# Kernel tuning notes

Measured on AMD Instinct MI355X. Metric: run time of the kernel, lower is better.

The kernel has to match this reference:

```python
import jax, jax.numpy as jnp
import numpy as np

N_NODES = 50000
IN_CH = 128
HID = 32
HEADS = 4
OUT_CH = 32
N_EDGES = 1600000
NEG_SLOPE = 0.2


def _gatv2(x, src, dst, Wl, bl, Wr, br, att, bias, H, C):
    """GATv2Conv (PyG semantics, add_self_loops already applied to src/dst).
    x: [N, F_in]; src/dst: [E]; Wl/Wr: [F_in, H*C]; att: [H, C]; bias: [H*C].
    Returns [N, H*C] (concat heads)."""
    N = x.shape[0]
    xl = (x @ Wl + bl).reshape(N, H, C)  # source-side transform
    xr = (x @ Wr + br).reshape(N, H, C)  # target-side transform
    e = jax.nn.leaky_relu(xl[src] + xr[dst], NEG_SLOPE)  # [E, H, C]
    logits = jnp.einsum('ehc,hc->eh', e, att)  # [E, H]
    # softmax over incoming edges of each target node (stable)
    m = jax.ops.segment_max(logits, dst, num_segments=N)[dst]
    p = jnp.exp(logits - m)
    denom = jax.ops.segment_sum(p, dst, num_segments=N)[dst]
    alpha = p / denom  # [E, H]
    out = jax.ops.segment_sum(alpha[:, :, None] * xl[src], dst, num_segments=N)
    return out.reshape(N, H * C) + bias


def setup_inputs() -> dict:
    key = jax.random.key(0)
    ks = jax.random.split(key, 16)
    s1 = 1.0 / np.sqrt(IN_CH)
    s2 = 1.0 / np.sqrt(HID * HEADS)
    inp = {
        'x': jax.random.normal(ks[0], (N_NODES, IN_CH), jnp.float32),
        'edge_index': jax.random.randint(ks[1], (2, N_EDGES), 0, N_NODES, jnp.int64 if jax.config.read('jax_enable_x64') else jnp.int32).astype(jnp.int32),
        # layer 1: in -> HID per head, HEADS heads
        'Wl1': jax.random.normal(ks[2], (IN_CH, HEADS * HID), jnp.float32) * s1,
        'bl1': jnp.zeros((HEADS * HID,), jnp.float32),
        'Wr1': jax.random.normal(ks[3], (IN_CH, HEADS * HID), jnp.float32) * s1,
        'br1': jnp.zeros((HEADS * HID,), jnp.float32),
        'att1': jax.random.normal(ks[4], (HEADS, HID), jnp.float32) * s1,
        'b1': jnp.zeros((HEADS * HID,), jnp.float32),
        # mu head: HID*HEADS -> OUT_CH, 1 head
        'Wl_mu': jax.random.normal(ks[5], (HEADS * HID, OUT_CH), jnp.float32) * s2,
        'bl_mu': jnp.zeros((OUT_CH,), jnp.float32),
        'Wr_mu': jax.random.normal(ks[6], (HEADS * HID, OUT_CH), jnp.float32) * s2,
        'br_mu': jnp.zeros((OUT_CH,), jnp.float32),
        'att_mu': jax.random.normal(ks[7], (1, OUT_CH), jnp.float32) * s2,
        'b_mu': jnp.zeros((OUT_CH,), jnp.float32),
        # logvar head
        'Wl_lv': jax.random.normal(ks[8], (HEADS * HID, OUT_CH), jnp.float32) * s2,
        'bl_lv': jnp.zeros((OUT_CH,), jnp.float32),
        'Wr_lv': jax.random.normal(ks[9], (HEADS * HID, OUT_CH), jnp.float32) * s2,
        'br_lv': jnp.zeros((OUT_CH,), jnp.float32),
        'att_lv': jax.random.normal(ks[10], (1, OUT_CH), jnp.float32) * s2,
        'b_lv': jnp.zeros((OUT_CH,), jnp.float32),
    }
    return inp


def reference(x, edge_index, Wl1, bl1, Wr1, br1, att1, b1,
              Wl_mu, bl_mu, Wr_mu, br_mu, att_mu, b_mu,
              Wl_lv, bl_lv, Wr_lv, br_lv, att_lv, b_lv):
    N = x.shape[0]
    loops = jnp.arange(N, dtype=edge_index.dtype)
    src = jnp.concatenate([edge_index[0], loops])  # add_self_loops=True
    dst = jnp.concatenate([edge_index[1], loops])
    h = jax.nn.relu(_gatv2(x, src, dst, Wl1, bl1, Wr1, br1, att1, b1, HEADS, HID))
    mu = _gatv2(h, src, dst, Wl_mu, bl_mu, Wr_mu, br_mu, att_mu, b_mu, 1, OUT_CH)
    logvar = _gatv2(h, src, dst, Wl_lv, bl_lv, Wr_lv, br_lv, att_lv, b_lv, 1, OUT_CH)
    return (mu, logvar)
```

## Files before the change

kernel.cpp:

```cpp
#include <hip/hip_runtime.h>
#include <hip/hip_fp16.h>

#define NNODES 50000
#define EORIG  1600000
#define ETOT   (EORIG + NNODES)
#define NEG 0.2f
#define BSH 7
#define NBUCK ((NNODES + 127) >> BSH)
#define BCAP 5120
#define NRT (NNODES / 16)
#define EPB 4096
#define LOG2E 1.44269504f

typedef _Float16 v2h __attribute__((ext_vector_type(2)));
typedef _Float16 v8h __attribute__((ext_vector_type(8)));
typedef float    v4f __attribute__((ext_vector_type(4)));

__device__ __forceinline__ float hdot2v(v2h a, v2h b, float c) {
#if __has_builtin(__builtin_amdgcn_fdot2)
    return __builtin_amdgcn_fdot2(a, b, c, false);
#else
    return c + (float)a.x * (float)b.x + (float)a.y * (float)b.y;
#endif
}

__device__ __forceinline__ float fexp2(float t) {
#if __has_builtin(__builtin_amdgcn_exp2f)
    return __builtin_amdgcn_exp2f(t);
#else
    return exp2f(t);
#endif
}

__global__ __launch_bounds__(256) void wcvt_kernel(
    const float* __restrict__ Wl, const float* __restrict__ Wr,
    const float* __restrict__ Wlmu, const float* __restrict__ Wllv,
    const float* __restrict__ Wrmu, const float* __restrict__ Wrlv,
    __half* __restrict__ WT, __half* __restrict__ WT2, int* __restrict__ bcur)
{
    int id = blockIdx.x * 256 + threadIdx.x;
    if (id < NBUCK) bcur[id] = 0;
    if (id < 32768) {
        int k = id >> 8, c = id & 255;
        float v = (c < 128) ? Wl[k * 128 + c] : Wr[k * 128 + (c - 128)];
        WT[c * 128 + k] = __float2half(v);
    } else if (id < 49152) {
        int loc = id - 32768;
        int k = loc >> 7, c = loc & 127;
        int sel = c >> 5, cc = c & 31;
        const float* W = sel == 0 ? Wlmu : sel == 1 ? Wllv : sel == 2 ? Wrmu : Wrlv;
        WT2[c * 128 + k] = __float2half(W[k * 32 + cc]);
    }
}

__global__ __launch_bounds__(256) void lin1_kernel(
    const float* __restrict__ x, const __half* __restrict__ WT,
    const float* __restrict__ bl, const float* __restrict__ br,
    __half* __restrict__ xl16, __half* __restrict__ xr16)
{
    int rt = (blockIdx.x * 256 + threadIdx.x) >> 6;
    if (rt >= NRT) return;
    int l  = threadIdx.x & 63;
    int lr = l & 15, lg = l >> 4;
    int row = rt * 16 + lr;

    v8h a[4];
    const float4* xrow = reinterpret_cast<const float4*>(x + (size_t)row * 128);
    #pragma unroll
    for (int ks = 0; ks < 4; ++ks) {
        float4 f0 = xrow[ks * 8 + lg * 2];
        float4 f1 = xrow[ks * 8 + lg * 2 + 1];
        v8h t;
        t[0]=(_Float16)f0.x; t[1]=(_Float16)f0.y; t[2]=(_Float16)f0.z; t[3]=(_Float16)f0.w;
        t[4]=(_Float16)f1.x; t[5]=(_Float16)f1.y; t[6]=(_Float16)f1.z; t[7]=(_Float16)f1.w;
        a[ks] = t;
    }

    const uint4* wt4 = reinterpret_cast<const uint4*>(WT);
    #pragma unroll 4
    for (int ct = 0; ct < 16; ++ct) {
        int c = ct * 16 + lr;
        v4f acc = {0.f, 0.f, 0.f, 0.f};
        #pragma unroll
        for (int ks = 0; ks < 4; ++ks) {
            union { uint4 u; v8h h; } B;
            B.u = wt4[(size_t)c * 16 + ks * 4 + lg];
            acc = __builtin_amdgcn_mfma_f32_16x16x32_f16(a[ks], B.h, acc, 0, 0, 0);
        }
        float bb = (c < 128) ? bl[c] : br[c - 128];
        #pragma unroll
        for (int j = 0; j < 4; ++j) {
            int orow = rt * 16 + lg * 4 + j;
            __half hv = __float2half(acc[j] + bb);
            if (c < 128) xl16[(size_t)orow * 128 + c] = hv;
            else         xr16[(size_t)orow * 128 + (c - 128)] = hv;
        }
    }
}

__global__ __launch_bounds__(256) void lin2_kernel(
    const __half* __restrict__ h16, const __half* __restrict__ WT2,
    const float* __restrict__ blmu, const float* __restrict__ bllv,
    const float* __restrict__ brmu, const float* __restrict__ brlv,
    __half* __restrict__ xi16, __half* __restrict__ xrI16)
{
    int rt = (blockIdx.x * 256 + threadIdx.x) >> 6;
    if (rt >= NRT) return;
    int l  = threadIdx.x & 63;
    int lr = l & 15, lg = l >> 4;
    int row = rt * 16 + lr;

    v8h a[4];
    const uint4* hrow = reinterpret_cast<const uint4*>(h16 + (size_t)row * 128);
    #pragma unroll
    for (int ks = 0; ks < 4; ++ks) {
        union { uint4 u; v8h h; } A;
        A.u = hrow[ks * 4 + lg];
        a[ks] = A.h;
    }

    const uint4* wt4 = reinterpret_cast<const uint4*>(WT2);
    #pragma unroll 4
    for (int ct = 0; ct < 8; ++ct) {
        int c = ct * 16 + lr;
        v4f acc = {0.f, 0.f, 0.f, 0.f};
        #pragma unroll
        for (int ks = 0; ks < 4; ++ks) {
            union { uint4 u; v8h h; } B;
            B.u = wt4[(size_t)c * 16 + ks * 4 + lg];
            acc = __builtin_amdgcn_mfma_f32_16x16x32_f16(a[ks], B.h, acc, 0, 0, 0);
        }
        int sel = c >> 5, cc = c & 31;
        const float* bp = sel == 0 ? blmu : sel == 1 ? bllv : sel == 2 ? brmu : brlv;
        float bb = bp[cc];
        #pragma unroll
        for (int j = 0; j < 4; ++j) {
            int orow = rt * 16 + lg * 4 + j;
            __half hv = __float2half(acc[j] + bb);
            if (c < 64) xi16 [(size_t)orow * 64 + c]      = hv;
            else        xrI16[(size_t)orow * 64 + (c-64)] = hv;
        }
    }
}

__global__ __launch_bounds__(256) void part_kernel(
    const int* __restrict__ src, const int* __restrict__ dst,
    int* __restrict__ bcur, unsigned int* __restrict__ pairs)
{
    __shared__ int cnt[NBUCK];
    __shared__ int gbase[NBUCK];
    const int e0 = blockIdx.x * EPB;

    for (int i = threadIdx.x; i < NBUCK; i += 256) cnt[i] = 0;
    __syncthreads();

    for (int i = threadIdx.x; i < EPB; i += 256) {
        int e = e0 + i;
        if (e >= ETOT) break;
        int d = (e < EORIG) ? dst[e] : e - EORIG;
        atomicAdd(&cnt[d >> BSH], 1);
    }
    __syncthreads();

    for (int b = threadIdx.x; b < NBUCK; b += 256) {
        int c = cnt[b];
        gbase[b] = c ? (b * BCAP + atomicAdd(&bcur[b], c)) : 0;
        cnt[b] = 0;
    }
    __syncthreads();

    for (int i = threadIdx.x; i < EPB; i += 256) {
        int e = e0 + i;
        if (e >= ETOT) break;
        int s, d;
        if (e < EORIG) { s = src[e]; d = dst[e]; }
        else           { s = d = e - EORIG; }
        int b = d >> BSH;
        int slot = atomicAdd(&cnt[b], 1);
        pairs[gbase[b] + slot] = (unsigned)s | ((unsigned)(d & 127) << 16);
    }
}

__global__ __launch_bounds__(256) void csrfill_kernel(
    const unsigned int* __restrict__ pairs, const int* __restrict__ bcur,
    int2* __restrict__ begend, unsigned short* __restrict__ csr)
{
    __shared__ int cnt[128];
    __shared__ int lofs[128];
    __shared__ int scnt[128];
    const int b = blockIdx.x, n0 = b << BSH;
    const int nn = min(128, NNODES - n0);
    const int pbase = b * BCAP;
    const int pend = pbase + bcur[b];
    const int t = threadIdx.x;

    if (t < 128) { cnt[t] = 0; scnt[t] = 0; }
    __syncthreads();
    for (int i = pbase + t; i < pend; i += 256)
        atomicAdd(&cnt[pairs[i] >> 16], 1);
    __syncthreads();

    if (t < 128) lofs[t] = cnt[t];
    __syncthreads();
    for (int off = 1; off < 128; off <<= 1) {
        int v = (t < 128 && t >= off) ? lofs[t - off] : 0;
        __syncthreads();
        if (t < 128) lofs[t] += v;
        __syncthreads();
    }
    if (t < 128) lofs[t] = pbase + lofs[t] - cnt[t];
    __syncthreads();

    if (t < nn) begend[n0 + t] = make_int2(lofs[t], lofs[t] + cnt[t]);

    for (int i = pbase + t; i < pend; i += 256) {
        unsigned pr = pairs[i];
        int l = pr >> 16;
        int slot = atomicAdd(&scnt[l], 1);
        csr[lofs[l] + slot] = (unsigned short)(pr & 0xFFFFu);
    }
}

__global__ __launch_bounds__(256) void gat_gather1(
    const __half* __restrict__ xl16, const __half* __restrict__ xr16,
    const float* __restrict__ att, const float* __restrict__ bias,
    const int2* __restrict__ begend, const unsigned short* __restrict__ csr,
    __half* __restrict__ h16)
{
    int d = (blockIdx.x * 256 + threadIdx.x) >> 6;
    if (d >= NNODES) return;
    int lane = threadIdx.x & 63;
    int quarter = lane >> 4;
    int q = lane & 15;
    int qo = quarter * 2;

    v2h xrh[4], ath[4];
    {
        union { uint4 u; v2h v[4]; } R;
        R.u = reinterpret_cast<const uint4*>(xr16)[(size_t)d * 16 + q];
        #pragma unroll
        for (int j = 0; j < 4; ++j) xrh[j] = R.v[j];
        const float4* t4 = reinterpret_cast<const float4*>(att) + q * 2;
        float4 a = t4[0], b = t4[1];
        ath[0] = (v2h){(_Float16)(a.x*LOG2E), (_Float16)(a.y*LOG2E)};
        ath[1] = (v2h){(_Float16)(a.z*LOG2E), (_Float16)(a.w*LOG2E)};
        ath[2] = (v2h){(_Float16)(b.x*LOG2E), (_Float16)(b.y*LOG2E)};
        ath[3] = (v2h){(_Float16)(b.z*LOG2E), (_Float16)(b.w*LOG2E)};
    }
    const v2h neg2 = (v2h){(_Float16)NEG, (_Float16)NEG};

    int2 be = begend[d];
    int beg = be.x, end = be.y;
    int nI = (end - beg + 7) >> 3;
    const uint4* xlu = reinterpret_cast<const uint4*>(xl16);

    float den = 0.f;
    float acc[8] = {0.f,0.f,0.f,0.f,0.f,0.f,0.f,0.f};

    auto compute = [&](uint4 U, bool val) {
        union { uint4 u; v2h v[4]; } X; X.u = U;
        float t = 0.f;
        #pragma unroll
        for (int j = 0; j < 4; ++j) {
            v2h s = X.v[j] + xrh[j];
            v2h l = __builtin_elementwise_max(s, s * neg2);
            t = hdot2v(l, ath[j], t);
        }
        t += __shfl_xor(t, 1, 64);
        t += __shfl_xor(t, 2, 64);
        float p = val ? fexp2(t) : 0.f;
        den += p;
        #pragma unroll
        for (int j = 0; j < 4; ++j) {
            acc[2*j]   += p * (float)X.v[j].x;
            acc[2*j+1] += p * (float)X.v[j].y;
        }
    };

    int  iA[2], iB[2], iC[2];
    bool vA[2], vB[2], vC[2];
    uint4 rA[2], rB[2];

    #pragma unroll
    for (int k = 0; k < 2; ++k) {
        int s = beg + qo + k;
        vA[k] = s < end;
        iA[k] = csr[vA[k] ? s : end - 1];
    }
    #pragma unroll
    for (int k = 0; k < 2; ++k) rA[k] = xlu[(size_t)iA[k] * 16 + q];
    #pragma unroll
    for (int k = 0; k < 2; ++k) {
        int s = beg + 8 + qo + k;
        vB[k] = s < end;
        iB[k] = csr[vB[k] ? s : end - 1];
    }
    #pragma unroll
    for (int k = 0; k < 2; ++k) rB[k] = xlu[(size_t)iB[k] * 16 + q];
    #pragma unroll
    for (int k = 0; k < 2; ++k) {
        int s = beg + 16 + qo + k;
        vC[k] = s < end;
        iC[k] = csr[vC[k] ? s : end - 1];
    }

    for (int it = 0; it < nI; ++it) {
        uint4 rC[2];
        #pragma unroll
        for (int k = 0; k < 2; ++k) rC[k] = xlu[(size_t)iC[k] * 16 + q];
        int b3 = beg + (it + 3) * 8;
        int iD[2]; bool vD[2];
        #pragma unroll
        for (int k = 0; k < 2; ++k) {
            int s = b3 + qo + k;
            vD[k] = s < end;
            iD[k] = csr[vD[k] ? s : end - 1];
        }
        compute(rA[0], vA[0]);
        compute(rA[1], vA[1]);
        #pragma unroll
        for (int k = 0; k < 2; ++k) {
            rA[k] = rB[k]; vA[k] = vB[k];
            rB[k] = rC[k]; vB[k] = vC[k];
            iC[k] = iD[k]; vC[k] = vD[k];
        }
    }

    den += __shfl_xor(den, 16, 64);
    den += __shfl_xor(den, 32, 64);
    #pragma unroll
    for (int j = 0; j < 8; ++j) {
        acc[j] += __shfl_xor(acc[j], 16, 64);
        acc[j] += __shfl_xor(acc[j], 32, 64);
    }

    if (quarter == 0) {
        float r = 1.f / den;
        const float4* bp = reinterpret_cast<const float4*>(bias) + q * 2;
        float4 ba = bp[0], bb = bp[1];
        __half hv[8];
        hv[0] = __float2half(fmaxf(acc[0]*r+ba.x, 0.f));
        hv[1] = __float2half(fmaxf(acc[1]*r+ba.y, 0.f));
        hv[2] = __float2half(fmaxf(acc[2]*r+ba.z, 0.f));
        hv[3] = __float2half(fmaxf(acc[3]*r+ba.w, 0.f));
        hv[4] = __float2half(fmaxf(acc[4]*r+bb.x, 0.f));
        hv[5] = __float2half(fmaxf(acc[5]*r+bb.y, 0.f));
        hv[6] = __float2half(fmaxf(acc[6]*r+bb.z, 0.f));
        hv[7] = __float2half(fmaxf(acc[7]*r+bb.w, 0.f));
        *reinterpret_cast<uint4*>(&h16[(size_t)d * 128 + q * 8]) =
            *reinterpret_cast<uint4*>(hv);
    }
}

__global__ __launch_bounds__(256) void gat_gather2(
    const __half* __restrict__ xi16, const __half* __restrict__ xrI16,
    const float* __restrict__ atmu, const float* __restrict__ atlv,
    const float* __restrict__ bmu,  const float* __restrict__ blv,
    const int2* __restrict__ begend, const unsigned short* __restrict__ csr,
    float* __restrict__ out)
{
    int d = (blockIdx.x * 256 + threadIdx.x) >> 6;
    if (d >= NNODES) return;
    int lane = threadIdx.x & 63;
    int oct = lane >> 3;
    int r   = lane & 7;
    bool lv = r >= 4;
    int cq  = lv ? r - 4 : r;
    int oo = oct * 2;

    v2h xrh[4], ath[4];
    {
        union { uint4 u; v2h v[4]; } R;
        R.u = reinterpret_cast<const uint4*>(xrI16)[(size_t)d * 8 + r];
        #pragma unroll
        for (int j = 0; j < 4; ++j) xrh[j] = R.v[j];
        const float4* t4 = reinterpret_cast<const float4*>(lv ? atlv : atmu) + cq * 2;
        float4 a = t4[0], b = t4[1];
        ath[0] = (v2h){(_Float16)(a.x*LOG2E), (_Float16)(a.y*LOG2E)};
        ath[1] = (v2h){(_Float16)(a.z*LOG2E), (_Float16)(a.w*LOG2E)};
        ath[2] = (v2h){(_Float16)(b.x*LOG2E), (_Float16)(b.y*LOG2E)};
        ath[3] = (v2h){(_Float16)(b.z*LOG2E), (_Float16)(b.w*LOG2E)};
    }
    const v2h neg2 = (v2h){(_Float16)NEG, (_Float16)NEG};

    int2 be = begend[d];
    int beg = be.x, end = be.y;
    int nI = (end - beg + 15) >> 4;
    const uint4* xiu = reinterpret_cast<const uint4*>(xi16);

    float den = 0.f;
    float acc[8] = {0.f,0.f,0.f,0.f,0.f,0.f,0.f,0.f};

    auto compute = [&](uint4 U, bool val) {
        union { uint4 u; v2h v[4]; } X; X.u = U;
        float t = 0.f;
        #pragma unroll
        for (int j = 0; j < 4; ++j) {
            v2h s = X.v[j] + xrh[j];
            v2h l = __builtin_elementwise_max(s, s * neg2);
            t = hdot2v(l, ath[j], t);
        }
        t += __shfl_xor(t, 1, 64);
        t += __shfl_xor(t, 2, 64);
        float p = val ? fexp2(t) : 0.f;
        den += p;
        #pragma unroll
        for (int j = 0; j < 4; ++j) {
            acc[2*j]   += p * (float)X.v[j].x;
            acc[2*j+1] += p * (float)X.v[j].y;
        }
    };

    int  iA[2], iB[2];
    bool vA[2], vB[2];
    uint4 rA[2];

    #pragma unroll
    for (int k = 0; k < 2; ++k) {
        int s = beg + oo + k;
        vA[k] = s < end;
        iA[k] = csr[vA[k] ? s : end - 1];
    }
    #pragma unroll
    for (int k = 0; k < 2; ++k) rA[k] = xiu[(size_t)iA[k] * 8 + r];
    #pragma unroll
    for (int k = 0; k < 2; ++k) {
        int s = beg + 16 + oo + k;
        vB[k] = s < end;
        iB[k] = csr[vB[k] ? s : end - 1];
    }

    for (int it = 0; it < nI; ++it) {
        int b2 = beg + (it + 2) * 16;
        int  iC[2]; bool vC[2];
        #pragma unroll
        for (int k = 0; k < 2; ++k) {
            int s = b2 + oo + k;
            vC[k] = s < end;
            iC[k] = csr[vC[k] ? s : end - 1];
        }
        uint4 rB[2];
        #pragma unroll
        for (int k = 0; k < 2; ++k) rB[k] = xiu[(size_t)iB[k] * 8 + r];
        #pragma unroll
        for (int k = 0; k < 2; ++k) compute(rA[k], vA[k]);
        #pragma unroll
        for (int k = 0; k < 2; ++k) {
            rA[k] = rB[k]; vA[k] = vB[k];
            iB[k] = iC[k]; vB[k] = vC[k];
        }
    }

    den += __shfl_xor(den, 8, 64);
    den += __shfl_xor(den, 16, 64);
    den += __shfl_xor(den, 32, 64);
    #pragma unroll
    for (int j = 0; j < 8; ++j) {
        acc[j] += __shfl_xor(acc[j], 8, 64);
        acc[j] += __shfl_xor(acc[j], 16, 64);
        acc[j] += __shfl_xor(acc[j], 32, 64);
    }

    if (oct == 0) {
        float rr = 1.f / den;
        const float4* bp = reinterpret_cast<const float4*>(lv ? blv : bmu) + cq * 2;
        float4 ba = bp[0], bb = bp[1];
        float4 o1 = make_float4(acc[0]*rr+ba.x, acc[1]*rr+ba.y,
                                acc[2]*rr+ba.z, acc[3]*rr+ba.w);
        float4 o2 = make_float4(acc[4]*rr+bb.x, acc[5]*rr+bb.y,
                                acc[6]*rr+bb.z, acc[7]*rr+bb.w);
        float* base_out = out + (lv ? 1600000 : 0);
        float4* op = reinterpret_cast<float4*>(base_out) + (size_t)d * 8 + cq * 2;
        op[0] = o1; op[1] = o2;
    }
}

extern "C" void kernel_launch(void* const* d_in, const int* in_sizes, int n_in,
                              void* d_out, int out_size, void* d_ws, size_t ws_size,
                              hipStream_t stream) {
    const float* x    = (const float*)d_in[0];
    const int*   ei   = (const int*)d_in[1];
    const float* Wl1  = (const float*)d_in[2];
    const float* bl1  = (const float*)d_in[3];
    const float* Wr1  = (const float*)d_in[4];
    const float* br1  = (const float*)d_in[5];
    const float* att1 = (const float*)d_in[6];
    const float* b1   = (const float*)d_in[7];
    const float* Wlmu = (const float*)d_in[8];
    const float* blmu = (const float*)d_in[9];
    const float* Wrmu = (const float*)d_in[10];
    const float* brmu = (const float*)d_in[11];
    const float* atmu = (const float*)d_in[12];
    const float* bmu  = (const float*)d_in[13];
    const float* Wllv = (const float*)d_in[14];
    const float* bllv = (const float*)d_in[15];
    const float* Wrlv = (const float*)d_in[16];
    const float* brlv = (const float*)d_in[17];
    const float* atlv = (const float*)d_in[18];
    const float* blv  = (const float*)d_in[19];

    float* out = (float*)d_out;
    float* ws  = (float*)d_ws;

    __half* xl16 = (__half*)ws;
    __half* xr16 = (__half*)(ws + 3200000);
    __half* h16  = (__half*)(ws + 6400000);
    __half* WT   = (__half*)(ws + 9600000);
    __half* WT2  = (__half*)(ws + 9620000);

    __half* xi16  = (__half*)ws;
    __half* xrI16 = (__half*)(ws + 1600000);

    int* ip = (int*)(ws + 10000000);
    unsigned int*   pairs  = (unsigned int*)ip;
    int*            bcur   = ip + 2001920;
    int2*           begend = (int2*)(ip + 2002312);
    unsigned short* csr    = (unsigned short*)(ip + 2102312);

    const int* srcp = ei;
    const int* dstp = ei + EORIG;

    const int NBE = (ETOT + EPB - 1) / EPB;

    wcvt_kernel<<<192, 256, 0, stream>>>(Wl1, Wr1, Wlmu, Wllv, Wrmu, Wrlv, WT, WT2, bcur);

    part_kernel<<<NBE, 256, 0, stream>>>(srcp, dstp, bcur, pairs);
    csrfill_kernel<<<NBUCK, 256, 0, stream>>>(pairs, bcur, begend, csr);

    lin1_kernel<<<(NRT + 3) / 4, 256, 0, stream>>>(x, WT, bl1, br1, xl16, xr16);

    gat_gather1<<<(NNODES * 64 + 255) / 256, 256, 0, stream>>>(
        xl16, xr16, att1, b1, begend, csr, h16);

    lin2_kernel<<<(NRT + 3) / 4, 256, 0, stream>>>(
        h16, WT2, blmu, bllv, brmu, brlv, xi16, xrI16);

    gat_gather2<<<(NNODES * 64 + 255) / 256, 256, 0, stream>>>(
        xi16, xrI16, atmu, atlv, bmu, blv, begend, csr, out);
}
```

Before: 196.8 us.

## Sort CSR neighbors by source range and shorten gather prefetch depth

The CSR fill kernel now counts and scans per (destination, source-high-bits) sub-bucket, so each node's neighbor list is grouped by source index range. This should give better locality in the later xl gathers. The layer-1 gather loop's software pipeline is cut from three stages of prefetch to two, which lowers register pressure but leaves less latency hiding. The larger shared arrays and the 256-wide scan add some cost to the fill kernel.

```diff
diff --git a/kernel.cpp b/kernel.cpp
--- a/kernel.cpp
+++ b/kernel.cpp
@@ -185,39 +185,54 @@
     const unsigned int* __restrict__ pairs, const int* __restrict__ bcur,
     int2* __restrict__ begend, unsigned short* __restrict__ csr)
 {
-    __shared__ int cnt[128];
-    __shared__ int lofs[128];
-    __shared__ int scnt[128];
+    __shared__ int cnt[1024];
+    __shared__ int pos[1024];
+    __shared__ int red[256];
     const int b = blockIdx.x, n0 = b << BSH;
     const int nn = min(128, NNODES - n0);
     const int pbase = b * BCAP;
     const int pend = pbase + bcur[b];
     const int t = threadIdx.x;
 
-    if (t < 128) { cnt[t] = 0; scnt[t] = 0; }
-    __syncthreads();
-    for (int i = pbase + t; i < pend; i += 256)
-        atomicAdd(&cnt[pairs[i] >> 16], 1);
-    __syncthreads();
-
-    if (t < 128) lofs[t] = cnt[t];
-    __syncthreads();
-    for (int off = 1; off < 128; off <<= 1) {
-        int v = (t < 128 && t >= off) ? lofs[t - off] : 0;
-        __syncthreads();
-        if (t < 128) lofs[t] += v;
-        __syncthreads();
-    }
-    if (t < 128) lofs[t] = pbase + lofs[t] - cnt[t];
-    __syncthreads();
-
-    if (t < nn) begend[n0 + t] = make_int2(lofs[t], lofs[t] + cnt[t]);
-
+    for (int i = t; i < 1024; i += 256) cnt[i] = 0;
+    __syncthreads();
     for (int i = pbase + t; i < pend; i += 256) {
         unsigned pr = pairs[i];
-        int l = pr >> 16;
-        int slot = atomicAdd(&scnt[l], 1);
-        csr[lofs[l] + slot] = (unsigned short)(pr & 0xFFFFu);
+        atomicAdd(&cnt[((pr >> 16) << 3) | ((pr & 0xFFFFu) >> 13)], 1);
+    }
+    __syncthreads();
+
+    int s0 = cnt[4*t], s1 = cnt[4*t+1], s2 = cnt[4*t+2], s3 = cnt[4*t+3];
+    int tot = s0 + s1 + s2 + s3;
+    red[t] = tot;
+    __syncthreads();
+    for (int off = 1; off < 256; off <<= 1) {
+        int v = (t >= off) ? red[t - off] : 0;
+        __syncthreads();
+        red[t] += v;
+        __syncthreads();
+    }
+    int excl = red[t] - tot;
+    pos[4*t]   = excl;
+    pos[4*t+1] = excl + s0;
+    pos[4*t+2] = excl + s0 + s1;
+    pos[4*t+3] = excl + s0 + s1 + s2;
+    __syncthreads();
+
+    if (t < nn) {
+        int bg = pbase + pos[t << 3];
+        int en = (t == 127) ? pend : pbase + pos[(t + 1) << 3];
+        begend[n0 + t] = make_int2(bg, en);
+    }
+
+    for (int i = t; i < 1024; i += 256) cnt[i] = 0;
+    __syncthreads();
+    for (int i = pbase + t; i < pend; i += 256) {
+        unsigned pr = pairs[i];
+        unsigned s = pr & 0xFFFFu;
+        int idx = ((pr >> 16) << 3) | (s >> 13);
+        int slot = atomicAdd(&cnt[idx], 1);
+        csr[pbase + pos[idx] + slot] = (unsigned short)s;
     }
 }
 
@@ -277,9 +292,9 @@
         }
     };
 
-    int  iA[2], iB[2], iC[2];
-    bool vA[2], vB[2], vC[2];
-    uint4 rA[2], rB[2];
+    int  iA[2], iB[2];
+    bool vA[2], vB[2];
+    uint4 rA[2];
 
     #pragma unroll
     for (int k = 0; k < 2; ++k) {
@@ -295,34 +310,25 @@
         vB[k] = s < end;
         iB[k] = csr[vB[k] ? s : end - 1];
     }
-    #pragma unroll
-    for (int k = 0; k < 2; ++k) rB[k] = xlu[(size_t)iB[k] * 16 + q];
-    #pragma unroll
-    for (int k = 0; k < 2; ++k) {
-        int s = beg + 16 + qo + k;
-        vC[k] = s < end;
-        iC[k] = csr[vC[k] ? s : end - 1];
-    }
 
     for (int it = 0; it < nI; ++it) {
-        uint4 rC[2];
-        #pragma unroll
-        for (int k = 0; k < 2; ++k) rC[k] = xlu[(size_t)iC[k] * 16 + q];
-        int b3 = beg + (it + 3) * 8;
-        int iD[2]; bool vD[2];
+        int b2 = beg + (it + 2) * 8;
+        int  iC[2]; bool vC[2];
         #pragma unroll
         for (int k = 0; k < 2; ++k) {
-            int s = b3 + qo + k;
-            vD[k] = s < end;
-            iD[k] = csr[vD[k] ? s : end - 1];
-        }
+            int s = b2 + qo + k;
+            vC[k] = s < end;
+            iC[k] = csr[vC[k] ? s : end - 1];
+        }
+        uint4 rB[2];
+        #pragma unroll
+        for (int k = 0; k < 2; ++k) rB[k] = xlu[(size_t)iB[k] * 16 + q];
         compute(rA[0], vA[0]);
         compute(rA[1], vA[1]);
         #pragma unroll
         for (int k = 0; k < 2; ++k) {
             rA[k] = rB[k]; vA[k] = vB[k];
-            rB[k] = rC[k]; vB[k] = vC[k];
-            iC[k] = iD[k]; vC[k] = vD[k];
+            iB[k] = iC[k]; vB[k] = vC[k];
         }
     }
 
```

Result: no change. 196.4 us (-0.2%).
